# Kernel optimization log

Measured on AMD Instinct MI355X. Metric: run time of the kernel, lower is better.

Reference implementation:

```python
import jax, jax.numpy as jnp
import numpy as np

NUM_NODES = 2000
B = 8
N = B * NUM_NODES          # 16000 total nodes
IN = 128                   # input feature dim
H, C = 4, 32               # heads, per-head out channels
HC = H * C                 # 128
DEG = 32
E = N * DEG                # 512000 edges
NEG = 0.2                  # leaky_relu negative slope (GATv2 default)
EPS = 1e-5
FC1, FC2, OUT = 512, 128, 1
MS = 3 * NUM_NODES         # fc_input_dim = num_nodes * len(which_layer)


def setup_inputs() -> dict:
    key = jax.random.key(0)
    ks = jax.random.split(key, 30)
    x = jax.random.normal(ks[0], (N, IN), jnp.float32)
    # intra-graph random edges: per-graph indices + graph offset
    src = jax.random.randint(ks[1], (B, NUM_NODES * DEG), 0, NUM_NODES)
    dst = jax.random.randint(ks[2], (B, NUM_NODES * DEG), 0, NUM_NODES)
    off = (jnp.arange(B) * NUM_NODES)[:, None]
    edge_index = jnp.stack([(src + off).reshape(-1), (dst + off).reshape(-1)]).astype(jnp.int64)

    def w(k, shape, fan_in):
        return (jax.random.normal(k, shape, jnp.float32) * (1.0 / np.sqrt(fan_in))).astype(jnp.float32)

    d = dict(x=x, edge_index=edge_index)
    # conv1: lin_l / lin_r (with bias), att [H,C], output bias [HC]
    d["Wl1"] = w(ks[3], (HC, IN), IN);  d["bl1"] = jnp.zeros((HC,), jnp.float32)
    d["Wr1"] = w(ks[4], (HC, IN), IN);  d["br1"] = jnp.zeros((HC,), jnp.float32)
    d["att1"] = w(ks[5], (H, C), C);    d["bias1"] = jnp.zeros((HC,), jnp.float32)
    # conv2 (input dim HC = 128)
    d["Wl2"] = w(ks[6], (HC, HC), HC);  d["bl2"] = jnp.zeros((HC,), jnp.float32)
    d["Wr2"] = w(ks[7], (HC, HC), HC);  d["br2"] = jnp.zeros((HC,), jnp.float32)
    d["att2"] = w(ks[8], (H, C), C);    d["bias2"] = jnp.zeros((HC,), jnp.float32)
    # pooling linears HC -> 1
    d["Wp1"] = w(ks[9], (1, HC), HC);   d["bp1"] = jnp.zeros((1,), jnp.float32)
    d["Wp2"] = w(ks[10], (1, HC), HC);  d["bp2"] = jnp.zeros((1,), jnp.float32)
    # layer norm over num_nodes
    d["ln_g"] = jnp.ones((NUM_NODES,), jnp.float32)
    d["ln_b"] = jnp.zeros((NUM_NODES,), jnp.float32)
    # fc encoder: MS -> 512 -> 128 -> 1
    d["We1"] = w(ks[11], (FC1, MS), MS);  d["be1"] = jnp.zeros((FC1,), jnp.float32)
    d["We2"] = w(ks[12], (FC2, FC1), FC1); d["be2"] = jnp.zeros((FC2,), jnp.float32)
    d["We3"] = w(ks[13], (OUT, FC2), FC2); d["be3"] = jnp.zeros((OUT,), jnp.float32)
    return d


def _gatv2(x, Wl, bl, Wr, br, att, bias, src, dst):
    # GATv2Conv (share_weights=False, concat=True), eval mode (no dropout)
    xl = (x @ Wl.T + bl).reshape(-1, H, C)   # messages (source side)
    xr = (x @ Wr.T + br).reshape(-1, H, C)   # destination side
    e = jax.nn.leaky_relu(xl[src] + xr[dst], NEG)          # [E_sl, H, C]
    a = jnp.einsum('ehc,hc->eh', e, att)                   # [E_sl, H]
    amax = jax.ops.segment_max(a, dst, num_segments=N)     # self-loops guarantee every dst is hit
    ex = jnp.exp(a - amax[dst])
    denom = jax.ops.segment_sum(ex, dst, num_segments=N)
    alpha = ex / denom[dst]                                # segment softmax per destination
    out = jax.ops.segment_sum(alpha[..., None] * xl[src], dst, num_segments=N)
    return out.reshape(N, HC) + bias


def _ln(v, g, b):
    m = v.mean(-1, keepdims=True)
    var = ((v - m) ** 2).mean(-1, keepdims=True)
    return (v - m) * jax.lax.rsqrt(var + EPS) * g + b


def reference(x, edge_index, Wl1, bl1, Wr1, br1, att1, bias1,
              Wl2, bl2, Wr2, br2, att2, bias2,
              Wp1, bp1, Wp2, bp2, ln_g, ln_b,
              We1, be1, We2, be2, We3, be3):
    loops = jnp.arange(N, dtype=edge_index.dtype)
    src = jnp.concatenate([edge_index[0], loops])  # add_self_loops=True
    dst = jnp.concatenate([edge_index[1], loops])

    x0 = x.mean(-1).reshape(B, NUM_NODES)          # to_dense_batch(mean(x,-1))
    h = jax.nn.relu(_gatv2(x, Wl1, bl1, Wr1, br1, att1, bias1, src, dst))
    x1 = (h @ Wp1.T + bp1).reshape(B, NUM_NODES)
    h = jax.nn.relu(_gatv2(h, Wl2, bl2, Wr2, br2, att2, bias2, src, dst))
    x2 = (h @ Wp2.T + bp2).reshape(B, NUM_NODES)

    x0 = _ln(x0, ln_g, ln_b); x1 = _ln(x1, ln_g, ln_b); x2 = _ln(x2, ln_g, ln_b)
    ms = jnp.concatenate([x0, x1, x2], axis=1)     # [B, 3*num_nodes]

    z = jax.nn.relu(ms @ We1.T + be1)
    z = jax.nn.relu(z @ We2.T + be2)
    pred = z @ We3.T + be3                         # [B, 1]
    return pred
```

## Files before the change

### kernel.cpp

```cpp
#include <hip/hip_runtime.h>

#define N_NODES 16000
#define NODES_G 2000
#define BATCH 8
#define INF 128
#define HCDIM 128
#define E_IN 512000
#define E_SL 528000
#define CAP 96
#define LSTRIDE 100
#define NEG_SLOPE 0.2f
#define LN_EPS 1e-5f
#define MS_DIM 6000
#define FC1_DIM 512
#define FC2_DIM 128

__global__ __launch_bounds__(256) void x0z_kernel(const float* __restrict__ x,
                                                  float* __restrict__ ms, int* __restrict__ cnt) {
    int tid = blockIdx.x * 256 + threadIdx.x;
    if (tid < N_NODES) cnt[tid] = 0;
    int wid = tid >> 6;
    int lane = tid & 63;
    float v = x[wid * INF + lane] + x[wid * INF + 64 + lane];
    #pragma unroll
    for (int off = 32; off > 0; off >>= 1) v += __shfl_xor(v, off, 64);
    if (lane == 0) {
        int b = wid / NODES_G, i = wid % NODES_G;
        ms[b * MS_DIM + i] = v * (1.0f / INF);
    }
}

__global__ __launch_bounds__(256) void scatter_kernel(const int* __restrict__ ei,
                                                      int* __restrict__ cnt, ushort* __restrict__ csrc) {
    int e = blockIdx.x * 256 + threadIdx.x;
    if (e >= E_SL) return;
    int s, d;
    if (e < E_IN) { s = ei[e]; d = ei[E_IN + e]; }
    else { s = e - E_IN; d = s; }
    int pos = atomicAdd(&cnt[d], 1);
    if (pos < CAP) csrc[d * CAP + pos] = (ushort)s;
}

__global__ __launch_bounds__(256) void gemm_dual_kernel(
    const float* __restrict__ X,
    const float* __restrict__ W1, const float* __restrict__ b1,
    const float* __restrict__ W2, const float* __restrict__ b2,
    float* __restrict__ out1, float* __restrict__ out2) {
    __shared__ float xs[32 * 128];
    int t = threadIdx.x;
    int row0 = blockIdx.x * 32;
    const float4* src = reinterpret_cast<const float4*>(X + (size_t)row0 * HCDIM);
    float4* dst = reinterpret_cast<float4*>(xs);
    #pragma unroll
    for (int i = 0; i < 4; ++i) dst[t + i * 256] = src[t + i * 256];
    __syncthreads();
    int col = t & 127;
    int half = t >> 7;
    const float* W = half ? W2 : W1;
    float bv = (half ? b2 : b1)[col];
    float* outp = half ? out2 : out1;
    float acc[32];
    #pragma unroll
    for (int r = 0; r < 32; ++r) acc[r] = 0.f;
    for (int k0 = 0; k0 < 128; k0 += 4) {
        float4 w4 = *reinterpret_cast<const float4*>(W + col * HCDIM + k0);
        #pragma unroll
        for (int r = 0; r < 32; ++r) {
            acc[r] += xs[r * 128 + k0] * w4.x + xs[r * 128 + k0 + 1] * w4.y
                    + xs[r * 128 + k0 + 2] * w4.z + xs[r * 128 + k0 + 3] * w4.w;
        }
    }
    #pragma unroll
    for (int r = 0; r < 32; ++r) outp[(size_t)(row0 + r) * HCDIM + col] = acc[r] + bv;
}

__global__ __launch_bounds__(256) void gat_node_kernel(
    const float* __restrict__ xl, const float* __restrict__ xr,
    const int* __restrict__ cnt, const ushort* __restrict__ csrc,
    const float* __restrict__ att, const float* __restrict__ bias,
    const float* __restrict__ Wp, const float* __restrict__ bp,
    float* __restrict__ hout, float* __restrict__ msout) {
    int n = blockIdx.x;
    int t = threadIdx.x;
    int g = t >> 5;
    int c = t & 31;
    int head = c >> 3;

    __shared__ int   csrc_s[CAP];
    __shared__ float as_[4 * LSTRIDE];
    __shared__ float rden_s[4];
    __shared__ float part[8 * 128];
    __shared__ float wred[2];

    int deg = cnt[n];
    int degc = deg < CAP ? deg : CAP;

    if (t < degc) csrc_s[t] = (int)csrc[n * CAP + t];
    __syncthreads();

    float4 att4 = *reinterpret_cast<const float4*>(att + 4 * c);
    float4 xr4  = *reinterpret_cast<const float4*>(xr + (size_t)n * HCDIM + 4 * c);

    float4 cache[8];
    #pragma unroll
    for (int it = 0; it < 8; ++it) {
        int j = g + 8 * it;
        if (j < degc) {
            int src = csrc_s[j];
            float4 v = *reinterpret_cast<const float4*>(xl + (size_t)src * HCDIM + 4 * c);
            cache[it] = v;
            float e0 = v.x + xr4.x; e0 = e0 > 0.f ? e0 : NEG_SLOPE * e0;
            float e1 = v.y + xr4.y; e1 = e1 > 0.f ? e1 : NEG_SLOPE * e1;
            float e2 = v.z + xr4.z; e2 = e2 > 0.f ? e2 : NEG_SLOPE * e2;
            float e3 = v.w + xr4.w; e3 = e3 > 0.f ? e3 : NEG_SLOPE * e3;
            float p = e0 * att4.x + e1 * att4.y + e2 * att4.z + e3 * att4.w;
            p += __shfl_xor(p, 1); p += __shfl_xor(p, 2); p += __shfl_xor(p, 4);
            if ((c & 7) == 0) as_[head * LSTRIDE + j] = p;
        }
    }
    for (int j = g + 64; j < degc; j += 8) {
        int src = csrc_s[j];
        float4 v = *reinterpret_cast<const float4*>(xl + (size_t)src * HCDIM + 4 * c);
        float e0 = v.x + xr4.x; e0 = e0 > 0.f ? e0 : NEG_SLOPE * e0;
        float e1 = v.y + xr4.y; e1 = e1 > 0.f ? e1 : NEG_SLOPE * e1;
        float e2 = v.z + xr4.z; e2 = e2 > 0.f ? e2 : NEG_SLOPE * e2;
        float e3 = v.w + xr4.w; e3 = e3 > 0.f ? e3 : NEG_SLOPE * e3;
        float p = e0 * att4.x + e1 * att4.y + e2 * att4.z + e3 * att4.w;
        p += __shfl_xor(p, 1); p += __shfl_xor(p, 2); p += __shfl_xor(p, 4);
        if ((c & 7) == 0) as_[head * LSTRIDE + j] = p;
    }
    __syncthreads();

    if (t < 128) {
        int h = t >> 5, s = t & 31;
        float m = -1e30f;
        for (int j = s; j < degc; j += 32) m = fmaxf(m, as_[h * LSTRIDE + j]);
        #pragma unroll
        for (int o = 16; o > 0; o >>= 1) m = fmaxf(m, __shfl_xor(m, o));
        float dsum = 0.f;
        for (int j = s; j < degc; j += 32) {
            float e = __expf(as_[h * LSTRIDE + j] - m);
            as_[h * LSTRIDE + j] = e;
            dsum += e;
        }
        #pragma unroll
        for (int o = 16; o > 0; o >>= 1) dsum += __shfl_xor(dsum, o);
        if (s == 0) rden_s[h] = 1.0f / dsum;
    }
    __syncthreads();

    float rden = rden_s[head];
    float ax = 0.f, ay = 0.f, az = 0.f, aw = 0.f;
    #pragma unroll
    for (int it = 0; it < 8; ++it) {
        int j = g + 8 * it;
        if (j < degc) {
            float a = as_[head * LSTRIDE + j] * rden;
            ax += a * cache[it].x; ay += a * cache[it].y;
            az += a * cache[it].z; aw += a * cache[it].w;
        }
    }
    for (int j = g + 64; j < degc; j += 8) {
        int src = csrc_s[j];
        float4 v = *reinterpret_cast<const float4*>(xl + (size_t)src * HCDIM + 4 * c);
        float a = as_[head * LSTRIDE + j] * rden;
        ax += a * v.x; ay += a * v.y; az += a * v.z; aw += a * v.w;
    }
    float4* pp = reinterpret_cast<float4*>(part + g * 128 + 4 * c);
    *pp = make_float4(ax, ay, az, aw);
    __syncthreads();

    if (t < 128) {
        float o = 0.f;
        #pragma unroll
        for (int gg = 0; gg < 8; ++gg) o += part[gg * 128 + t];
        o += bias[t];
        o = fmaxf(o, 0.f);
        hout[(size_t)n * HCDIM + t] = o;

        float p = o * Wp[t];
        #pragma unroll
        for (int off = 32; off > 0; off >>= 1) p += __shfl_xor(p, off, 64);
        if ((t & 63) == 0) wred[t >> 6] = p;
    }
    __syncthreads();
    if (t == 0) {
        int b = n / NODES_G, i = n % NODES_G;
        msout[b * MS_DIM + i] = wred[0] + wred[1] + bp[0];
    }
}

__global__ __launch_bounds__(256) void ln_kernel(float* __restrict__ ms,
                                                 const float* __restrict__ g, const float* __restrict__ bta) {
    int b = blockIdx.x / 3, st = blockIdx.x % 3;
    float* row = ms + b * MS_DIM + st * NODES_G;
    int t = threadIdx.x;
    float s = 0.f, ss = 0.f;
    for (int j = t; j < NODES_G; j += 256) { float v = row[j]; s += v; ss += v * v; }
    __shared__ float rs_[4], rss[4];
    #pragma unroll
    for (int off = 32; off > 0; off >>= 1) { s += __shfl_xor(s, off, 64); ss += __shfl_xor(ss, off, 64); }
    int w = t >> 6, lane = t & 63;
    if (lane == 0) { rs_[w] = s; rss[w] = ss; }
    __syncthreads();
    s = rs_[0] + rs_[1] + rs_[2] + rs_[3];
    ss = rss[0] + rss[1] + rss[2] + rss[3];
    float mean = s * (1.0f / NODES_G);
    float var = ss * (1.0f / NODES_G) - mean * mean;
    float rstd = rsqrtf(var + LN_EPS);
    for (int j = t; j < NODES_G; j += 256) {
        float v = row[j];
        row[j] = (v - mean) * rstd * g[j] + bta[j];
    }
}

template<int K, int OD, bool RELU>
__global__ __launch_bounds__(256) void fcb_kernel(const float* __restrict__ in, const float* __restrict__ W,
                                                  const float* __restrict__ bias, float* __restrict__ z) {
    int o = blockIdx.x;
    int t = threadIdx.x;
    const float* wrow = W + (size_t)o * K;
    float acc[8];
    #pragma unroll
    for (int b = 0; b < 8; ++b) acc[b] = 0.f;
    for (int k = t; k < K; k += 256) {
        float wv = wrow[k];
        #pragma unroll
        for (int b = 0; b < 8; ++b) acc[b] += wv * in[b * K + k];
    }
    #pragma unroll
    for (int off = 32; off > 0; off >>= 1)
        #pragma unroll
        for (int b = 0; b < 8; ++b) acc[b] += __shfl_xor(acc[b], off, 64);
    __shared__ float red[4][8];
    int w = t >> 6, lane = t & 63;
    if (lane == 0) {
        #pragma unroll
        for (int b = 0; b < 8; ++b) red[w][b] = acc[b];
    }
    __syncthreads();
    if (t < 8) {
        float v = red[0][t] + red[1][t] + red[2][t] + red[3][t] + bias[o];
        z[t * OD + o] = RELU ? fmaxf(v, 0.f) : v;
    }
}

__global__ __launch_bounds__(256) void fc3_kernel(const float* __restrict__ z2, const float* __restrict__ W,
                                                  const float* __restrict__ bias, float* __restrict__ out) {
    int t = threadIdx.x;
    int b = t >> 5, l = t & 31;
    float acc = 0.f;
    #pragma unroll
    for (int i = 0; i < 4; ++i) {
        int k = l + i * 32;
        acc += z2[b * FC2_DIM + k] * W[k];
    }
    #pragma unroll
    for (int off = 16; off > 0; off >>= 1) acc += __shfl_xor(acc, off, 32);
    if (l == 0) out[b] = acc + bias[0];
}

extern "C" void kernel_launch(void* const* d_in, const int* in_sizes, int n_in,
                              void* d_out, int out_size, void* d_ws, size_t ws_size,
                              hipStream_t stream) {
    const float* x    = (const float*)d_in[0];
    const int*   ei   = (const int*)d_in[1];
    const float* Wl1  = (const float*)d_in[2];
    const float* bl1  = (const float*)d_in[3];
    const float* Wr1  = (const float*)d_in[4];
    const float* br1  = (const float*)d_in[5];
    const float* att1 = (const float*)d_in[6];
    const float* bias1= (const float*)d_in[7];
    const float* Wl2  = (const float*)d_in[8];
    const float* bl2  = (const float*)d_in[9];
    const float* Wr2  = (const float*)d_in[10];
    const float* br2  = (const float*)d_in[11];
    const float* att2 = (const float*)d_in[12];
    const float* bias2= (const float*)d_in[13];
    const float* Wp1  = (const float*)d_in[14];
    const float* bp1  = (const float*)d_in[15];
    const float* Wp2  = (const float*)d_in[16];
    const float* bp2  = (const float*)d_in[17];
    const float* ln_g = (const float*)d_in[18];
    const float* ln_b = (const float*)d_in[19];
    const float* We1  = (const float*)d_in[20];
    const float* be1  = (const float*)d_in[21];
    const float* We2  = (const float*)d_in[22];
    const float* be2  = (const float*)d_in[23];
    const float* We3  = (const float*)d_in[24];
    const float* be3  = (const float*)d_in[25];
    float* out = (float*)d_out;

    float* ws = (float*)d_ws;
    float* xl = ws;
    float* xr = xl + (size_t)N_NODES * HCDIM;
    float* hb = xr + (size_t)N_NODES * HCDIM;
    float* ms = hb + (size_t)N_NODES * HCDIM;
    float* z1 = ms + BATCH * MS_DIM;
    float* z2 = z1 + BATCH * FC1_DIM;
    int* cnt  = (int*)(z2 + BATCH * FC2_DIM);
    ushort* csrc = (ushort*)(cnt + N_NODES);

    int eb = (E_SL + 255) / 256;
    x0z_kernel<<<N_NODES / 4, 256, 0, stream>>>(x, ms, cnt);
    scatter_kernel<<<eb, 256, 0, stream>>>(ei, cnt, csrc);

    gemm_dual_kernel<<<N_NODES / 32, 256, 0, stream>>>(x, Wl1, bl1, Wr1, br1, xl, xr);
    gat_node_kernel<<<N_NODES, 256, 0, stream>>>(xl, xr, cnt, csrc, att1, bias1, Wp1, bp1, hb, ms + 2000);
    gemm_dual_kernel<<<N_NODES / 32, 256, 0, stream>>>(hb, Wl2, bl2, Wr2, br2, xl, xr);
    gat_node_kernel<<<N_NODES, 256, 0, stream>>>(xl, xr, cnt, csrc, att2, bias2, Wp2, bp2, hb, ms + 4000);

    ln_kernel<<<24, 256, 0, stream>>>(ms, ln_g, ln_b);
    fcb_kernel<MS_DIM, FC1_DIM, true><<<FC1_DIM, 256, 0, stream>>>(ms, We1, be1, z1);
    fcb_kernel<FC1_DIM, FC2_DIM, true><<<FC2_DIM, 256, 0, stream>>>(z1, We2, be2, z2);
    fc3_kernel<<<1, 256, 0, stream>>>(z2, We3, be3, out);
}
```

Measured before the change: 317.4 us.

## Retile dual GEMM to 16-row blocks with 2x8 register tiles per thread

The dual projection GEMM now handles 16 rows per block instead of 32. Each thread computes a 2-row by 8-column register tile using float4 reads from shared memory and vectorized float4 stores. Previously each thread did 32 rows by one column with scalar broadcast LDS reads. The aim is fewer LDS reads per FMA, more blocks for occupancy, and coalesced vector stores. In exchange, each thread now reads its weights from global or L1 with a strided per-thread pattern, where lanes touch rows 8 apart.

```diff
diff --git a/kernel.cpp b/kernel.cpp
--- a/kernel.cpp
+++ b/kernel.cpp
@@ -46,32 +46,54 @@
     const float* __restrict__ W1, const float* __restrict__ b1,
     const float* __restrict__ W2, const float* __restrict__ b2,
     float* __restrict__ out1, float* __restrict__ out2) {
-    __shared__ float xs[32 * 128];
-    int t = threadIdx.x;
-    int row0 = blockIdx.x * 32;
+    __shared__ float xs[16 * 128];
+    int t = threadIdx.x;
+    int row0 = blockIdx.x * 16;
     const float4* src = reinterpret_cast<const float4*>(X + (size_t)row0 * HCDIM);
     float4* dst = reinterpret_cast<float4*>(xs);
-    #pragma unroll
-    for (int i = 0; i < 4; ++i) dst[t + i * 256] = src[t + i * 256];
-    __syncthreads();
-    int col = t & 127;
-    int half = t >> 7;
-    const float* W = half ? W2 : W1;
-    float bv = (half ? b2 : b1)[col];
-    float* outp = half ? out2 : out1;
-    float acc[32];
-    #pragma unroll
-    for (int r = 0; r < 32; ++r) acc[r] = 0.f;
-    for (int k0 = 0; k0 < 128; k0 += 4) {
-        float4 w4 = *reinterpret_cast<const float4*>(W + col * HCDIM + k0);
-        #pragma unroll
-        for (int r = 0; r < 32; ++r) {
-            acc[r] += xs[r * 128 + k0] * w4.x + xs[r * 128 + k0 + 1] * w4.y
-                    + xs[r * 128 + k0 + 2] * w4.z + xs[r * 128 + k0 + 3] * w4.w;
+    dst[t] = src[t];
+    dst[t + 256] = src[t + 256];
+    __syncthreads();
+
+    int cg = t & 31;
+    int rg = t >> 5;
+    int colBase = cg * 8;
+    bool second = colBase >= 128;
+    const float* W  = second ? W2 : W1;
+    const float* bb = second ? b2 : b1;
+    float* outp     = second ? out2 : out1;
+    int lc = colBase - (second ? 128 : 0);
+
+    float acc0[8], acc1[8];
+    #pragma unroll
+    for (int j = 0; j < 8; ++j) { acc0[j] = 0.f; acc1[j] = 0.f; }
+
+    const float4* xs4 = reinterpret_cast<const float4*>(xs);
+    const float4* wbase = reinterpret_cast<const float4*>(W + (size_t)lc * HCDIM);
+
+    for (int k4 = 0; k4 < 32; ++k4) {
+        float4 xa = xs4[(rg * 2 + 0) * 32 + k4];
+        float4 xb = xs4[(rg * 2 + 1) * 32 + k4];
+        #pragma unroll
+        for (int j = 0; j < 8; ++j) {
+            float4 w = wbase[j * 32 + k4];
+            acc0[j] += xa.x * w.x + xa.y * w.y + xa.z * w.z + xa.w * w.w;
+            acc1[j] += xb.x * w.x + xb.y * w.y + xb.z * w.z + xb.w * w.w;
         }
     }
-    #pragma unroll
-    for (int r = 0; r < 32; ++r) outp[(size_t)(row0 + r) * HCDIM + col] = acc[r] + bv;
+
+    float4 bv0 = *reinterpret_cast<const float4*>(bb + lc);
+    float4 bv1 = *reinterpret_cast<const float4*>(bb + lc + 4);
+    int r0 = row0 + rg * 2;
+    float4 o;
+    o = make_float4(acc0[0] + bv0.x, acc0[1] + bv0.y, acc0[2] + bv0.z, acc0[3] + bv0.w);
+    *reinterpret_cast<float4*>(outp + (size_t)r0 * HCDIM + lc) = o;
+    o = make_float4(acc0[4] + bv1.x, acc0[5] + bv1.y, acc0[6] + bv1.z, acc0[7] + bv1.w);
+    *reinterpret_cast<float4*>(outp + (size_t)r0 * HCDIM + lc + 4) = o;
+    o = make_float4(acc1[0] + bv0.x, acc1[1] + bv0.y, acc1[2] + bv0.z, acc1[3] + bv0.w);
+    *reinterpret_cast<float4*>(outp + (size_t)(r0 + 1) * HCDIM + lc) = o;
+    o = make_float4(acc1[4] + bv1.x, acc1[5] + bv1.y, acc1[6] + bv1.z, acc1[7] + bv1.w);
+    *reinterpret_cast<float4*>(outp + (size_t)(r0 + 1) * HCDIM + lc + 4) = o;
 }
 
 __global__ __launch_bounds__(256) void gat_node_kernel(
@@ -305,9 +327,9 @@
     x0z_kernel<<<N_NODES / 4, 256, 0, stream>>>(x, ms, cnt);
     scatter_kernel<<<eb, 256, 0, stream>>>(ei, cnt, csrc);
 
-    gemm_dual_kernel<<<N_NODES / 32, 256, 0, stream>>>(x, Wl1, bl1, Wr1, br1, xl, xr);
+    gemm_dual_kernel<<<N_NODES / 16, 256, 0, stream>>>(x, Wl1, bl1, Wr1, br1, xl, xr);
     gat_node_kernel<<<N_NODES, 256, 0, stream>>>(xl, xr, cnt, csrc, att1, bias1, Wp1, bp1, hb, ms + 2000);
-    gemm_dual_kernel<<<N_NODES / 32, 256, 0, stream>>>(hb, Wl2, bl2, Wr2, br2, xl, xr);
+    gemm_dual_kernel<<<N_NODES / 16, 256, 0, stream>>>(hb, Wl2, bl2, Wr2, br2, xl, xr);
     gat_node_kernel<<<N_NODES, 256, 0, stream>>>(xl, xr, cnt, csrc, att2, bias2, Wp2, bp2, hb, ms + 4000);
 
     ln_kernel<<<24, 256, 0, stream>>>(ms, ln_g, ln_b);
```

New measurement: 486.8 us. +53.4%, slower.
